# Kernel optimization log

Hardware: AMD Instinct MI355X
Metric: run time of the kernel (lower is better)

## Reference

```python
import jax, jax.numpy as jnp
import numpy as np

B, S, D, H, E, K = 1, 4096, 1024, 4096, 8, 2


def setup_inputs() -> dict:
    key = jax.random.key(0)
    ks = jax.random.split(key, 10)
    scale = 0.02
    return {
        "hidden_states": jax.random.normal(ks[0], (B, S, D), dtype=jnp.float32),
        "gate_w": jax.random.normal(ks[1], (E, D), dtype=jnp.float32) * scale,
        "w_in": jax.random.normal(ks[2], (E, D, H), dtype=jnp.float32) * scale,
        "b_in": jnp.zeros((E, H), dtype=jnp.float32),
        "w_out": jax.random.normal(ks[3], (E, H, D), dtype=jnp.float32) * scale,
        "b_out": jnp.zeros((E, D), dtype=jnp.float32),
        "sw_in": jax.random.normal(ks[4], (D, H), dtype=jnp.float32) * scale,
        "sb_in": jnp.zeros((H,), dtype=jnp.float32),
        "sw_out": jax.random.normal(ks[5], (H, D), dtype=jnp.float32) * scale,
        "sb_out": jnp.zeros((D,), dtype=jnp.float32),
    }


def _ffn(x, w1, b1, w2, b2):
    # Linear -> exact (erf) GELU -> Linear, matching torch F.gelu default
    h = jax.nn.gelu(x @ w1 + b1, approximate=False)
    return h @ w2 + b2


def reference(hidden_states, gate_w, w_in, b_in, w_out, b_out,
              sw_in, sb_in, sw_out, sb_out):
    orig_shape = hidden_states.shape
    d = orig_shape[-1]
    x = hidden_states.reshape(-1, d)            # [T, D]
    T = x.shape[0]
    n_exp = gate_w.shape[0]

    # --- MoE gate: softmax over expert logits, top-k (sorted flag irrelevant
    # since the combine below is order-invariant) ---
    scores = jax.nn.softmax(x @ gate_w.T, axis=-1)        # [T, E]
    topk_w, topk_idx = jax.lax.top_k(scores, K)           # [T, K]

    # Per-token dense combine weights: w_tok[t, e] = sum of topk weights routed to e
    w_tok = jnp.zeros((T, n_exp), dtype=x.dtype).at[
        jnp.arange(T)[:, None], topk_idx].add(topk_w)     # [T, E]

    # --- expert dispatch + weighted combine (loop over small fixed E) ---
    y = jnp.zeros_like(x)
    for e in range(n_exp):
        y = y + w_tok[:, e:e + 1] * _ffn(x, w_in[e], b_in[e], w_out[e], b_out[e])

    # --- shared expert on the full (unflattened) input ---
    shared = _ffn(hidden_states, sw_in, sb_in, sw_out, sb_out)
    return y.reshape(orig_shape) + shared
```

## Files before the change

kernel.cpp:

```cpp
#include <hip/hip_runtime.h>
#include <hip/hip_bf16.h>
#include <math.h>


typedef unsigned short ushort_t;
typedef __attribute__((ext_vector_type(8))) __bf16 bf16x8;
typedef __attribute__((ext_vector_type(4))) float f32x4;

#define T_TOK 4096
#define DDIM  1024
#define HDIM  4096
#define NEXP  8
#define SLOT_MAX 9216
#define M_ALL (SLOT_MAX + T_TOK)

#define OFF_CNT   0u
#define OFF_OFFS  64u
#define OFF_TIDX  256u
#define OFF_TW    33024u
#define OFF_SLOT  65792u
#define OFF_TOK   98560u
#define OFF_XALL  1048576u
#define OFF_OUTS  OFF_XALL
#define OFF_WT    (OFF_XALL + 28311552u)
#define OFF_H     (OFF_WT + 75497472u)

__device__ __forceinline__ ushort_t f2b(float f) {
    __hip_bfloat16 h = __float2bfloat16(f);
    return *reinterpret_cast<ushort_t*>(&h);
}
__device__ __forceinline__ float b2f(ushort_t u) {
    __hip_bfloat16 h;
    *reinterpret_cast<ushort_t*>(&h) = u;
    return __bfloat162float(h);
}
__device__ __forceinline__ float gelu_exact(float v) {
    return 0.5f * v * (1.0f + erff(v * 0.70710678118654752f));
}

__global__ void init_kernel(int* __restrict__ cnt, int* __restrict__ tok_of) {
    int i = blockIdx.x * 256 + threadIdx.x;
    if (i < 16) cnt[i] = 0;
    if (i < SLOT_MAX) tok_of[i] = -1;
}

__global__ void gate_kernel(const float* __restrict__ x, const float* __restrict__ gw,
                            int* __restrict__ tidx, float* __restrict__ tw,
                            int* __restrict__ cnt) {
    int t = blockIdx.x;
    int l = threadIdx.x;
    float acc[NEXP];
#pragma unroll
    for (int e = 0; e < NEXP; ++e) acc[e] = 0.f;
    for (int i = 0; i < DDIM / 64; ++i) {
        float xi = x[(size_t)t * DDIM + i * 64 + l];
#pragma unroll
        for (int e = 0; e < NEXP; ++e)
            acc[e] += xi * gw[e * DDIM + i * 64 + l];
    }
#pragma unroll
    for (int e = 0; e < NEXP; ++e)
        for (int off = 32; off; off >>= 1) acc[e] += __shfl_xor(acc[e], off);
    if (l == 0) {
        float m = acc[0];
#pragma unroll
        for (int e = 1; e < NEXP; ++e) m = fmaxf(m, acc[e]);
        float ex[NEXP], Z = 0.f;
#pragma unroll
        for (int e = 0; e < NEXP; ++e) { ex[e] = __expf(acc[e] - m); Z += ex[e]; }
        int b0 = 0;
#pragma unroll
        for (int e = 1; e < NEXP; ++e) if (ex[e] > ex[b0]) b0 = e;
        int b1 = (b0 == 0) ? 1 : 0;
#pragma unroll
        for (int e = 0; e < NEXP; ++e) if (e != b0 && ex[e] > ex[b1]) b1 = e;
        float inv = 1.0f / Z;
        tidx[2 * t] = b0; tidx[2 * t + 1] = b1;
        tw[2 * t] = ex[b0] * inv; tw[2 * t + 1] = ex[b1] * inv;
        atomicAdd(&cnt[b0], 1);
        atomicAdd(&cnt[b1], 1);
    }
}

__global__ void offs_kernel(const int* __restrict__ cnt, int* __restrict__ offs) {
    if (threadIdx.x == 0 && blockIdx.x == 0) {
        int o = 0;
#pragma unroll
        for (int e = 0; e < NEXP; ++e) {
            offs[e] = o;
            o += (cnt[e] + 127) & ~127;
        }
        offs[NEXP] = o;
    }
}

__global__ void assign_kernel(const int* __restrict__ tidx, const int* __restrict__ offs,
                              int* __restrict__ cur, int* __restrict__ slot_of,
                              int* __restrict__ tok_of) {
    int i = blockIdx.x * 256 + threadIdx.x;
    if (i >= 2 * T_TOK) return;
    int e = tidx[i];
    int s = offs[e] + atomicAdd(&cur[e], 1);
    slot_of[i] = s;
    tok_of[s] = i >> 1;
}

__global__ void build_x(const float* __restrict__ x, const int* __restrict__ tok_of,
                        const int* __restrict__ offs, ushort_t* __restrict__ Xall) {
    int b = blockIdx.x;
    int k = threadIdx.x * 4;
    int t;
    if (b < SLOT_MAX) {
        if (b >= offs[NEXP]) return;
        t = tok_of[b];
    } else {
        t = b - SLOT_MAX;
    }
    float4 v = make_float4(0.f, 0.f, 0.f, 0.f);
    if (t >= 0) v = *(const float4*)(x + (size_t)t * DDIM + k);
    ushort_t* p = Xall + (size_t)b * DDIM + k;
    p[0] = f2b(v.x); p[1] = f2b(v.y); p[2] = f2b(v.z); p[3] = f2b(v.w);
}

__global__ void transpose_cvt(const float* __restrict__ in, ushort_t* __restrict__ out,
                              int K, int N) {
    __shared__ float t[64][65];
    size_t zoff = (size_t)blockIdx.z * K * N;
    in += zoff; out += zoff;
    int k0 = blockIdx.x * 64, n0 = blockIdx.y * 64;
    int c = threadIdx.x & 63, r4 = threadIdx.x >> 6;
#pragma unroll
    for (int i = 0; i < 16; ++i) {
        int r = r4 + i * 4;
        t[r][c] = in[(size_t)(k0 + r) * N + n0 + c];
    }
    __syncthreads();
#pragma unroll
    for (int i = 0; i < 16; ++i) {
        int r = r4 + i * 4;
        out[(size_t)(n0 + r) * K + k0 + c] = f2b(t[c][r]);
    }
}

template <bool ACT_GELU, bool FFN2>
__global__ __launch_bounds__(256) void gemm_moe(
    const ushort_t* __restrict__ A, const ushort_t* __restrict__ WtBase,
    const float* __restrict__ bExp, const float* __restrict__ bSh,
    ushort_t* __restrict__ Cb, float* __restrict__ Cf,
    const int* __restrict__ offs, int N, int K) {
    int m0 = blockIdx.x * 128, n0 = blockIdx.y * 128;
    int e;
    if (m0 >= SLOT_MAX) {
        e = NEXP;
    } else {
        if (m0 >= offs[NEXP]) return;
        e = 0;
        while (offs[e + 1] <= m0) e++;
    }
    const ushort_t* Bt = WtBase + (size_t)e * N * K;
    const float* bias = (e == NEXP) ? bSh : bExp + (size_t)e * N;

    __shared__ ushort_t As[2][128 * 64];
    __shared__ ushort_t Bs[2][128 * 64];

    int tid = threadIdx.x;
    int lane = tid & 63, wid = tid >> 6;
    int wm = wid >> 1, wn = wid & 1;
    int q = lane >> 4, lr = lane & 15;

    size_t Aoff[4], Boff[4];
    int ldsOff[4];
#pragma unroll
    for (int it = 0; it < 4; ++it) {
        int row = it * 32 + (tid >> 3);
        int c = (tid & 7) ^ (row & 7);
        Aoff[it] = (size_t)(m0 + row) * K + c * 8;
        Boff[it] = (size_t)(n0 + row) * K + c * 8;
        ldsOff[it] = (it * 256 + wid * 64) * 8;
    }

    int rowA[4], rowB[4];
#pragma unroll
    for (int i = 0; i < 4; ++i) {
        rowA[i] = wm * 64 + i * 16 + lr;
        rowB[i] = wn * 64 + i * 16 + lr;
    }

    f32x4 acc[4][4];
#pragma unroll
    for (int i = 0; i < 4; ++i)
#pragma unroll
        for (int j = 0; j < 4; ++j) acc[i][j] = (f32x4)(0.f);

    auto stage = [&](int kb, int buf) {
#pragma unroll
        for (int it = 0; it < 4; ++it) {
            __builtin_amdgcn_global_load_lds(
                (const __attribute__((address_space(1))) void*)(A + Aoff[it] + kb),
                (__attribute__((address_space(3))) void*)(&As[buf][ldsOff[it]]), 16, 0, 0);
            __builtin_amdgcn_global_load_lds(
                (const __attribute__((address_space(1))) void*)(Bt + Boff[it] + kb),
                (__attribute__((address_space(3))) void*)(&Bs[buf][ldsOff[it]]), 16, 0, 0);
        }
    };
    auto compute = [&](int buf) {
#pragma unroll
        for (int ks = 0; ks < 2; ++ks) {
            bf16x8 af[4], bfr[4];
#pragma unroll
            for (int i = 0; i < 4; ++i) {
                int cA = (ks * 4 + q) ^ (rowA[i] & 7);
                af[i] = *(const bf16x8*)(&As[buf][rowA[i] * 64 + cA * 8]);
                int cB = (ks * 4 + q) ^ (rowB[i] & 7);
                bfr[i] = *(const bf16x8*)(&Bs[buf][rowB[i] * 64 + cB * 8]);
            }
#pragma unroll
            for (int i = 0; i < 4; ++i)
#pragma unroll
                for (int j = 0; j < 4; ++j)
                    acc[i][j] = __builtin_amdgcn_mfma_f32_16x16x32_bf16(
                        af[i], bfr[j], acc[i][j], 0, 0, 0);
        }
    };

    const int nk = K >> 6;
    stage(0, 0);
    __syncthreads();
    int cur = 0;
    for (int t = 0; t < nk; ++t) {
        if (t + 1 < nk) stage((t + 1) << 6, cur ^ 1);
        compute(cur);
        __syncthreads();
        cur ^= 1;
    }

    int colb = n0 + wn * 64 + lr;
    int rowb = m0 + wm * 64 + q * 4;
#pragma unroll
    for (int j = 0; j < 4; ++j) {
        int col = colb + j * 16;
        float bz = bias[col];
#pragma unroll
        for (int i = 0; i < 4; ++i) {
            int row = rowb + i * 16;
#pragma unroll
            for (int r = 0; r < 4; ++r) {
                float v = acc[i][j][r] + bz;
                if (ACT_GELU) v = gelu_exact(v);
                if (!FFN2 || e < NEXP)
                    Cb[(size_t)(row + r) * N + col] = f2b(v);
                else
                    Cf[(size_t)(row + r - SLOT_MAX) * N + col] = v;
            }
        }
    }
}

__global__ void combine_kernel(float* __restrict__ out, const ushort_t* __restrict__ OutS,
                               const int* __restrict__ slot_of, const float* __restrict__ tw) {
    int t = blockIdx.x;
    int d = threadIdx.x * 4;
    int s0 = slot_of[2 * t], s1 = slot_of[2 * t + 1];
    float w0 = tw[2 * t], w1 = tw[2 * t + 1];
    float* po = out + (size_t)t * DDIM + d;
    float4 o = *(float4*)po;
    const ushort_t* p0 = OutS + (size_t)s0 * DDIM + d;
    const ushort_t* p1 = OutS + (size_t)s1 * DDIM + d;
    o.x += w0 * b2f(p0[0]) + w1 * b2f(p1[0]);
    o.y += w0 * b2f(p0[1]) + w1 * b2f(p1[1]);
    o.z += w0 * b2f(p0[2]) + w1 * b2f(p1[2]);
    o.w += w0 * b2f(p0[3]) + w1 * b2f(p1[3]);
    *(float4*)po = o;
}

extern "C" void kernel_launch(void* const* d_in, const int* in_sizes, int n_in,
                              void* d_out, int out_size, void* d_ws, size_t ws_size,
                              hipStream_t stream) {
    const float* x      = (const float*)d_in[0];
    const float* gw     = (const float*)d_in[1];
    const float* w_in   = (const float*)d_in[2];
    const float* b_in   = (const float*)d_in[3];
    const float* w_out  = (const float*)d_in[4];
    const float* b_out  = (const float*)d_in[5];
    const float* sw_in  = (const float*)d_in[6];
    const float* sb_in  = (const float*)d_in[7];
    const float* sw_out = (const float*)d_in[8];
    const float* sb_out = (const float*)d_in[9];
    float* out = (float*)d_out;

    char* ws = (char*)d_ws;
    int*      cnt     = (int*)(ws + OFF_CNT);
    int*      offs    = (int*)(ws + OFF_OFFS);
    int*      tidx    = (int*)(ws + OFF_TIDX);
    float*    tw      = (float*)(ws + OFF_TW);
    int*      slot_of = (int*)(ws + OFF_SLOT);
    int*      tok_of  = (int*)(ws + OFF_TOK);
    ushort_t* Xall    = (ushort_t*)(ws + OFF_XALL);
    ushort_t* OutS    = (ushort_t*)(ws + OFF_OUTS);
    ushort_t* Wt      = (ushort_t*)(ws + OFF_WT);
    ushort_t* Hbuf    = (ushort_t*)(ws + OFF_H);

    init_kernel<<<(SLOT_MAX + 255) / 256, 256, 0, stream>>>(cnt, tok_of);
    gate_kernel<<<T_TOK, 64, 0, stream>>>(x, gw, tidx, tw, cnt);
    offs_kernel<<<1, 64, 0, stream>>>(cnt, offs);
    assign_kernel<<<(2 * T_TOK + 255) / 256, 256, 0, stream>>>(tidx, offs, cnt + 8,
                                                               slot_of, tok_of);
    build_x<<<M_ALL, 256, 0, stream>>>(x, tok_of, offs, Xall);

    transpose_cvt<<<dim3(DDIM / 64, HDIM / 64, NEXP), 256, 0, stream>>>(w_in, Wt, DDIM, HDIM);
    transpose_cvt<<<dim3(DDIM / 64, HDIM / 64, 1), 256, 0, stream>>>(
        sw_in, Wt + (size_t)NEXP * HDIM * DDIM, DDIM, HDIM);
    gemm_moe<true, false><<<dim3(M_ALL / 128, HDIM / 128), 256, 0, stream>>>(
        Xall, Wt, b_in, sb_in, Hbuf, nullptr, offs, HDIM, DDIM);

    transpose_cvt<<<dim3(HDIM / 64, DDIM / 64, NEXP), 256, 0, stream>>>(w_out, Wt, HDIM, DDIM);
    transpose_cvt<<<dim3(HDIM / 64, DDIM / 64, 1), 256, 0, stream>>>(
        sw_out, Wt + (size_t)NEXP * HDIM * DDIM, HDIM, DDIM);
    gemm_moe<false, true><<<dim3(M_ALL / 128, DDIM / 128), 256, 0, stream>>>(
        Hbuf, Wt, b_out, sb_out, OutS, out, offs, DDIM, HDIM);

    combine_kernel<<<T_TOK, 256, 0, stream>>>(out, OutS, slot_of, tw);
    (void)in_sizes; (void)n_in; (void)out_size; (void)ws_size;
}
```

Baseline: 636.0 us.

## Use 256x256 tiles with 8-wave blocks, XCD-aware remap and staggered pipelining

Replaces the 128x128, 4-wave grouped GEMM with a 256x256 tile computed by 512 threads (8 waves, each 128x64). Work-group indices are remapped so neighbouring tiles land on the same XCD. The loop is restructured so A and B loads are staged at different points with explicit vmcnt/lgkmcnt waits, barriers and setprio around MFMA bursts. Expert segment padding goes up to 256 rows to match the larger M tile. Each block now reuses more data, but the extra padding rows add wasted work and fewer blocks may leave parts of the GPU idle on the smaller second GEMM.

```diff
diff --git a/kernel.cpp b/kernel.cpp
--- a/kernel.cpp
+++ b/kernel.cpp
@@ -11,8 +11,8 @@
 #define DDIM  1024
 #define HDIM  4096
 #define NEXP  8
-#define SLOT_MAX 9216
-#define M_ALL (SLOT_MAX + T_TOK)
+#define SLOT_PAD 10240
+#define M_ALL (SLOT_PAD + T_TOK)
 
 #define OFF_CNT   0u
 #define OFF_OFFS  64u
@@ -22,7 +22,7 @@
 #define OFF_TOK   98560u
 #define OFF_XALL  1048576u
 #define OFF_OUTS  OFF_XALL
-#define OFF_WT    (OFF_XALL + 28311552u)
+#define OFF_WT    (OFF_XALL + 29360128u)
 #define OFF_H     (OFF_WT + 75497472u)
 
 __device__ __forceinline__ ushort_t f2b(float f) {
@@ -41,7 +41,7 @@
 __global__ void init_kernel(int* __restrict__ cnt, int* __restrict__ tok_of) {
     int i = blockIdx.x * 256 + threadIdx.x;
     if (i < 16) cnt[i] = 0;
-    if (i < SLOT_MAX) tok_of[i] = -1;
+    if (i < SLOT_PAD) tok_of[i] = -1;
 }
 
 __global__ void gate_kernel(const float* __restrict__ x, const float* __restrict__ gw,
@@ -88,7 +88,7 @@
 #pragma unroll
         for (int e = 0; e < NEXP; ++e) {
             offs[e] = o;
-            o += (cnt[e] + 127) & ~127;
+            o += (cnt[e] + 255) & ~255;
         }
         offs[NEXP] = o;
     }
@@ -110,11 +110,11 @@
     int b = blockIdx.x;
     int k = threadIdx.x * 4;
     int t;
-    if (b < SLOT_MAX) {
+    if (b < SLOT_PAD) {
         if (b >= offs[NEXP]) return;
         t = tok_of[b];
     } else {
-        t = b - SLOT_MAX;
+        t = b - SLOT_PAD;
     }
     float4 v = make_float4(0.f, 0.f, 0.f, 0.f);
     if (t >= 0) v = *(const float4*)(x + (size_t)t * DDIM + k);
@@ -143,14 +143,23 @@
 }
 
 template <bool ACT_GELU, bool FFN2>
-__global__ __launch_bounds__(256) void gemm_moe(
+__global__ __launch_bounds__(512, 2) void gemm_moe8(
     const ushort_t* __restrict__ A, const ushort_t* __restrict__ WtBase,
     const float* __restrict__ bExp, const float* __restrict__ bSh,
     ushort_t* __restrict__ Cb, float* __restrict__ Cf,
     const int* __restrict__ offs, int N, int K) {
-    int m0 = blockIdx.x * 128, n0 = blockIdx.y * 128;
+    int MT = gridDim.x;
+    int nwg = MT * gridDim.y;
+    int flat = blockIdx.y * MT + blockIdx.x;
+    int q8 = nwg >> 3;
+    int idx = (flat & 7) * q8 + (flat >> 3);
+    int pairsz = MT * 2;
+    int pp = idx / pairsz, rr = idx % pairsz;
+    int m0 = (rr >> 1) * 256;
+    int n0 = (pp * 2 + (rr & 1)) * 256;
+
     int e;
-    if (m0 >= SLOT_MAX) {
+    if (m0 >= SLOT_PAD) {
         e = NEXP;
     } else {
         if (m0 >= offs[NEXP]) return;
@@ -160,97 +169,142 @@
     const ushort_t* Bt = WtBase + (size_t)e * N * K;
     const float* bias = (e == NEXP) ? bSh : bExp + (size_t)e * N;
 
-    __shared__ ushort_t As[2][128 * 64];
-    __shared__ ushort_t Bs[2][128 * 64];
+    __shared__ ushort_t As[2][2][128 * 64];
+    __shared__ ushort_t Bs[2][2][128 * 64];
 
     int tid = threadIdx.x;
     int lane = tid & 63, wid = tid >> 6;
-    int wm = wid >> 1, wn = wid & 1;
-    int q = lane >> 4, lr = lane & 15;
-
-    size_t Aoff[4], Boff[4];
-    int ldsOff[4];
-#pragma unroll
-    for (int it = 0; it < 4; ++it) {
-        int row = it * 32 + (tid >> 3);
-        int c = (tid & 7) ^ (row & 7);
-        Aoff[it] = (size_t)(m0 + row) * K + c * 8;
-        Boff[it] = (size_t)(n0 + row) * K + c * 8;
-        ldsOff[it] = (it * 256 + wid * 64) * 8;
-    }
-
-    int rowA[4], rowB[4];
-#pragma unroll
-    for (int i = 0; i < 4; ++i) {
-        rowA[i] = wm * 64 + i * 16 + lr;
-        rowB[i] = wn * 64 + i * 16 + lr;
-    }
-
-    f32x4 acc[4][4];
-#pragma unroll
-    for (int i = 0; i < 4; ++i)
+    int wm = wid >> 2, wn = wid & 3;
+    int q4 = lane >> 4, lr = lane & 15;
+
+    unsigned aoff[2][2], boff[2][2];
+    int ldsL[2];
+#pragma unroll
+    for (int i = 0; i < 2; ++i) {
+        int L = i * 512 + tid;
+        int row = L >> 3;
+        int csrc = (L & 7) ^ (row & 7);
+        ldsL[i] = L * 8;
+#pragma unroll
+        for (int h = 0; h < 2; ++h) {
+            aoff[h][i] = (unsigned)(m0 + h * 128 + row) * (unsigned)K + csrc * 8;
+            boff[h][i] = (unsigned)(n0 + h * 128 + row) * (unsigned)K + csrc * 8;
+        }
+    }
+
+    auto stageA = [&](int kbb, int sb) {
+#pragma unroll
+        for (int h = 0; h < 2; ++h)
+#pragma unroll
+            for (int i = 0; i < 2; ++i)
+                __builtin_amdgcn_global_load_lds(
+                    (const __attribute__((address_space(1))) void*)(A + aoff[h][i] + kbb),
+                    (__attribute__((address_space(3))) void*)(&As[sb][h][ldsL[i]]), 16, 0, 0);
+    };
+    auto stageB = [&](int kbb, int sb) {
+#pragma unroll
+        for (int h = 0; h < 2; ++h)
+#pragma unroll
+            for (int i = 0; i < 2; ++i)
+                __builtin_amdgcn_global_load_lds(
+                    (const __attribute__((address_space(1))) void*)(Bt + boff[h][i] + kbb),
+                    (__attribute__((address_space(3))) void*)(&Bs[sb][h][ldsL[i]]), 16, 0, 0);
+    };
+
+    f32x4 acc[8][4];
+#pragma unroll
+    for (int i = 0; i < 8; ++i)
 #pragma unroll
         for (int j = 0; j < 4; ++j) acc[i][j] = (f32x4)(0.f);
 
-    auto stage = [&](int kb, int buf) {
-#pragma unroll
-        for (int it = 0; it < 4; ++it) {
-            __builtin_amdgcn_global_load_lds(
-                (const __attribute__((address_space(1))) void*)(A + Aoff[it] + kb),
-                (__attribute__((address_space(3))) void*)(&As[buf][ldsOff[it]]), 16, 0, 0);
-            __builtin_amdgcn_global_load_lds(
-                (const __attribute__((address_space(1))) void*)(Bt + Boff[it] + kb),
-                (__attribute__((address_space(3))) void*)(&Bs[buf][ldsOff[it]]), 16, 0, 0);
+    bf16x8 bfr[4][2];
+    int lx = lr & 7;
+    int bcol = (wn & 1) * 64 + lr;
+
+    auto read_af = [&](const ushort_t* Ah, int mi0, bf16x8 af[2][2]) {
+#pragma unroll
+        for (int d = 0; d < 2; ++d)
+#pragma unroll
+            for (int ks = 0; ks < 2; ++ks) {
+                int c = ((ks << 2) + q4) ^ lx;
+                af[d][ks] = *(const bf16x8*)(Ah + ((mi0 + d) * 16 + lr) * 64 + c * 8);
+            }
+    };
+    auto mma_body = [&](int mi0, bf16x8 af[2][2]) {
+        asm volatile("s_waitcnt lgkmcnt(0)" ::: "memory");
+        __builtin_amdgcn_sched_barrier(0);
+        __builtin_amdgcn_s_setprio(1);
+#pragma unroll
+        for (int d = 0; d < 2; ++d)
+#pragma unroll
+            for (int nj = 0; nj < 4; ++nj)
+#pragma unroll
+                for (int ks = 0; ks < 2; ++ks)
+                    acc[mi0 + d][nj] = __builtin_amdgcn_mfma_f32_16x16x32_bf16(
+                        af[d][ks], bfr[nj][ks], acc[mi0 + d][nj], 0, 0, 0);
+        __builtin_amdgcn_s_setprio(0);
+        __builtin_amdgcn_s_barrier();
+    };
+
+    stageA(0, 0);
+    stageB(0, 0);
+
+    const int nk = K >> 6;
+    for (int t = 0; t < nk; ++t) {
+        int buf = t & 1;
+        int kb = (t + 1) << 6;
+        const ushort_t* Ah = As[buf][wm];
+        const ushort_t* Bh = Bs[buf][wn >> 1];
+        bf16x8 afA[2][2], afB[2][2];
+
+        if (t + 1 < nk) {
+            stageA(kb, buf ^ 1);
+            asm volatile("s_waitcnt vmcnt(4)" ::: "memory");
+        } else {
+            asm volatile("s_waitcnt vmcnt(0)" ::: "memory");
         }
-    };
-    auto compute = [&](int buf) {
-#pragma unroll
-        for (int ks = 0; ks < 2; ++ks) {
-            bf16x8 af[4], bfr[4];
-#pragma unroll
-            for (int i = 0; i < 4; ++i) {
-                int cA = (ks * 4 + q) ^ (rowA[i] & 7);
-                af[i] = *(const bf16x8*)(&As[buf][rowA[i] * 64 + cA * 8]);
-                int cB = (ks * 4 + q) ^ (rowB[i] & 7);
-                bfr[i] = *(const bf16x8*)(&Bs[buf][rowB[i] * 64 + cB * 8]);
+        __builtin_amdgcn_s_barrier();
+#pragma unroll
+        for (int nj = 0; nj < 4; ++nj)
+#pragma unroll
+            for (int ks = 0; ks < 2; ++ks) {
+                int c = ((ks << 2) + q4) ^ lx;
+                bfr[nj][ks] = *(const bf16x8*)(Bh + (bcol + nj * 16) * 64 + c * 8);
             }
-#pragma unroll
-            for (int i = 0; i < 4; ++i)
-#pragma unroll
-                for (int j = 0; j < 4; ++j)
-                    acc[i][j] = __builtin_amdgcn_mfma_f32_16x16x32_bf16(
-                        af[i], bfr[j], acc[i][j], 0, 0, 0);
-        }
-    };
-
-    const int nk = K >> 6;
-    stage(0, 0);
-    __syncthreads();
-    int cur = 0;
-    for (int t = 0; t < nk; ++t) {
-        if (t + 1 < nk) stage((t + 1) << 6, cur ^ 1);
-        compute(cur);
-        __syncthreads();
-        cur ^= 1;
-    }
-
-    int colb = n0 + wn * 64 + lr;
-    int rowb = m0 + wm * 64 + q * 4;
-#pragma unroll
-    for (int j = 0; j < 4; ++j) {
-        int col = colb + j * 16;
-        float bz = bias[col];
-#pragma unroll
-        for (int i = 0; i < 4; ++i) {
-            int row = rowb + i * 16;
+        read_af(Ah, 0, afA);
+        mma_body(0, afA);
+
+        read_af(Ah, 2, afB);
+        if (t + 1 < nk) stageB(kb, buf ^ 1);
+        __builtin_amdgcn_s_barrier();
+        mma_body(2, afB);
+
+        read_af(Ah, 4, afA);
+        __builtin_amdgcn_s_barrier();
+        mma_body(4, afA);
+
+        read_af(Ah, 6, afB);
+        __builtin_amdgcn_s_barrier();
+        mma_body(6, afB);
+    }
+
+    int rb = m0 + wm * 128 + q4 * 4;
+    int cb = n0 + wn * 64 + lr;
+#pragma unroll
+    for (int mi = 0; mi < 8; ++mi) {
+        int row = rb + mi * 16;
+#pragma unroll
+        for (int nj = 0; nj < 4; ++nj) {
+            int col = cb + nj * 16;
+            float bz = bias[col];
 #pragma unroll
             for (int r = 0; r < 4; ++r) {
-                float v = acc[i][j][r] + bz;
+                float v = acc[mi][nj][r] + bz;
                 if (ACT_GELU) v = gelu_exact(v);
                 if (!FFN2 || e < NEXP)
                     Cb[(size_t)(row + r) * N + col] = f2b(v);
                 else
-                    Cf[(size_t)(row + r - SLOT_MAX) * N + col] = v;
+                    Cf[(size_t)(row + r - SLOT_PAD) * N + col] = v;
             }
         }
     }
@@ -300,7 +354,7 @@
     ushort_t* Wt      = (ushort_t*)(ws + OFF_WT);
     ushort_t* Hbuf    = (ushort_t*)(ws + OFF_H);
 
-    init_kernel<<<(SLOT_MAX + 255) / 256, 256, 0, stream>>>(cnt, tok_of);
+    init_kernel<<<(SLOT_PAD + 255) / 256, 256, 0, stream>>>(cnt, tok_of);
     gate_kernel<<<T_TOK, 64, 0, stream>>>(x, gw, tidx, tw, cnt);
     offs_kernel<<<1, 64, 0, stream>>>(cnt, offs);
     assign_kernel<<<(2 * T_TOK + 255) / 256, 256, 0, stream>>>(tidx, offs, cnt + 8,
@@ -310,13 +364,13 @@
     transpose_cvt<<<dim3(DDIM / 64, HDIM / 64, NEXP), 256, 0, stream>>>(w_in, Wt, DDIM, HDIM);
     transpose_cvt<<<dim3(DDIM / 64, HDIM / 64, 1), 256, 0, stream>>>(
         sw_in, Wt + (size_t)NEXP * HDIM * DDIM, DDIM, HDIM);
-    gemm_moe<true, false><<<dim3(M_ALL / 128, HDIM / 128), 256, 0, stream>>>(
+    gemm_moe8<true, false><<<dim3(M_ALL / 256, HDIM / 256), 512, 0, stream>>>(
         Xall, Wt, b_in, sb_in, Hbuf, nullptr, offs, HDIM, DDIM);
 
     transpose_cvt<<<dim3(HDIM / 64, DDIM / 64, NEXP), 256, 0, stream>>>(w_out, Wt, HDIM, DDIM);
     transpose_cvt<<<dim3(HDIM / 64, DDIM / 64, 1), 256, 0, stream>>>(
         sw_out, Wt + (size_t)NEXP * HDIM * DDIM, HDIM, DDIM);
-    gemm_moe<false, true><<<dim3(M_ALL / 128, DDIM / 128), 256, 0, stream>>>(
+    gemm_moe8<false, true><<<dim3(M_ALL / 256, DDIM / 256), 512, 0, stream>>>(
         Hbuf, Wt, b_out, sb_out, OutS, out, offs, DDIM, HDIM);
 
     combine_kernel<<<T_TOK, 256, 0, stream>>>(out, OutS, slot_of, tw);
```

After: 680.3 us. +7.0%, slower.
